# Optimization experiments

Measured on AMD Instinct MI355X. Metric: run time of the kernel, lower is better.

Reference implementation:

```python
import jax, jax.numpy as jnp
import numpy as np

C = 256   # hidden_size (in_channels)
V = 97    # VOC_SIZE + 1
T = 32    # encoder time steps
N = 4096  # batch of text instances


def setup_inputs() -> dict:
    key = jax.random.key(0)
    ks = jax.random.split(key, 10)
    s = lambda k, shape: jax.random.normal(k, shape, dtype=jnp.float32) * 0.05
    return {
        "input": jax.random.randint(ks[0], (N,), 0, V),
        "hidden": s(ks[1], (1, N, C)),
        "encoder_outputs": s(ks[2], (T, N, C)),
        "emb": s(ks[3], (V, C)),
        "combine_w": s(ks[4], (C, 2 * C)), "combine_b": jnp.zeros((C,), jnp.float32),
        "vat_w": s(ks[5], (1, C)), "vat_b": jnp.zeros((1,), jnp.float32),
        "gru_w_ih": s(ks[6], (3 * C, C)), "gru_w_hh": s(ks[7], (3 * C, C)),
        "gru_b_ih": jnp.zeros((3 * C,), jnp.float32), "gru_b_hh": jnp.zeros((3 * C,), jnp.float32),
        "out_w": s(ks[8], (V, C)), "out_b": jnp.zeros((V,), jnp.float32),
    }


def reference(input, hidden, encoder_outputs, emb, combine_w, combine_b,
              vat_w, vat_b, gru_w_ih, gru_w_hh, gru_b_ih, gru_b_hh,
              out_w, out_b):
    # Embedding lookup (dropout = identity in eval mode)
    embedded = emb[input]                                   # [N, C]

    # Bahdanau additive attention: vat(tanh(hidden + enc))
    alpha = jnp.tanh(hidden + encoder_outputs)              # [T, N, C]
    scores = jnp.einsum('tnc,c->nt', alpha, vat_w[0]) + vat_b[0]  # [N, T]
    attn = jax.nn.softmax(scores, axis=1)                   # [N, T]
    applied = jnp.einsum('nt,tnc->nc', attn, encoder_outputs)     # [N, C]

    # Combine + relu
    x = jnp.concatenate([embedded, applied], axis=1) @ combine_w.T + combine_b  # [N, C]
    x = jax.nn.relu(x)

    # Single-step GRU cell (PyTorch gate ordering: r, z, n)
    h = hidden[0]                                           # [N, C]
    gi = x @ gru_w_ih.T + gru_b_ih                          # [N, 3C]
    gh = h @ gru_w_hh.T + gru_b_hh                          # [N, 3C]
    ir, iz, i_n = jnp.split(gi, 3, axis=1)
    hr, hz, h_n = jnp.split(gh, 3, axis=1)
    r = jax.nn.sigmoid(ir + hr)
    z = jax.nn.sigmoid(iz + hz)
    n = jnp.tanh(i_n + r * h_n)
    h_new = (1.0 - z) * n + z * h                           # [N, C]

    out = jax.nn.log_softmax(h_new @ out_w.T + out_b, axis=1)  # [N, V]
    return out, h_new[None, :, :], attn[:, None, :]
```

## Files before the change

### kernel.cpp

```cpp
#include <hip/hip_runtime.h>

typedef unsigned short u16;
typedef unsigned int u32;
using bf16x8 = __attribute__((ext_vector_type(8))) __bf16;
using f32x4  = __attribute__((ext_vector_type(4))) float;

__device__ __forceinline__ u16 f2bf(float f) {
  union { float f; unsigned int i; } v; v.f = f;
  unsigned int r = v.i + 0x7fffu + ((v.i >> 16) & 1u);
  return (u16)(r >> 16);
}
__device__ __forceinline__ void cvt8(u16* dst, const float* src) {
  float4 a0 = *reinterpret_cast<const float4*>(src);
  float4 a1 = *reinterpret_cast<const float4*>(src + 4);
  dst[0] = f2bf(a0.x); dst[1] = f2bf(a0.y); dst[2] = f2bf(a0.z); dst[3] = f2bf(a0.w);
  dst[4] = f2bf(a1.x); dst[5] = f2bf(a1.y); dst[6] = f2bf(a1.z); dst[7] = f2bf(a1.w);
}
__device__ __forceinline__ float ftanh(float x) {
  float e = __expf(2.f * x);
  return 1.f - 2.f / (e + 1.f);
}
__device__ __forceinline__ float fsigm(float x) {
  return 1.f / (1.f + __expf(-x));
}
__device__ __forceinline__ float ptanh(float x) {
  const float c1 = -0.3333333333f, c2 = 0.1333333333f, c3 = -0.0539682540f;
  float t = x * x;
  float r = __builtin_fmaf(__builtin_fmaf(c3, t, c2), t, c1);
  return __builtin_fmaf(x * t, r, x);
}

__global__ __launch_bounds__(512) void k_attn(
    const float* __restrict__ enc, const float* __restrict__ hid,
    const float* __restrict__ vw,
    const float* __restrict__ emb, const int* __restrict__ inp,
    float* __restrict__ attn_out, u16* __restrict__ Acomb)
{
  __shared__ float es_s[16 * 33];
  __shared__ float l_s[16];

  const int tid = threadIdx.x;
  const int nl  = tid >> 5;
  const int cg  = tid & 31;
  const int c0  = cg * 8;
  const int n   = blockIdx.x * 16 + nl;

  const float4 h0 = *reinterpret_cast<const float4*>(&hid[n * 256 + c0]);
  const float4 h1 = *reinterpret_cast<const float4*>(&hid[n * 256 + c0 + 4]);
  const float4 w0 = *reinterpret_cast<const float4*>(&vw[c0]);
  const float4 w1 = *reinterpret_cast<const float4*>(&vw[c0 + 4]);

  float a0=0.f,a1=0.f,a2=0.f,a3=0.f,a4=0.f,a5=0.f,a6=0.f,a7=0.f;
  float l = 0.f;

  const float* ep = &enc[(size_t)n * 256 + c0];
  #pragma unroll 4
  for (int t = 0; t < 32; ++t) {
    const float* p = ep + (size_t)t * 1048576;
    float4 e0 = *reinterpret_cast<const float4*>(p);
    float4 e1 = *reinterpret_cast<const float4*>(p + 4);

    float s;
    s  = ptanh(h0.x + e0.x) * w0.x;
    s  = __builtin_fmaf(ptanh(h0.y + e0.y), w0.y, s);
    s  = __builtin_fmaf(ptanh(h0.z + e0.z), w0.z, s);
    s  = __builtin_fmaf(ptanh(h0.w + e0.w), w0.w, s);
    s  = __builtin_fmaf(ptanh(h1.x + e1.x), w1.x, s);
    s  = __builtin_fmaf(ptanh(h1.y + e1.y), w1.y, s);
    s  = __builtin_fmaf(ptanh(h1.z + e1.z), w1.z, s);
    s  = __builtin_fmaf(ptanh(h1.w + e1.w), w1.w, s);
    #pragma unroll
    for (int k = 16; k >= 1; k >>= 1) s += __shfl_xor(s, k, 64);

    float e = __expf(s);
    l += e;
    a0 = __builtin_fmaf(e, e0.x, a0); a1 = __builtin_fmaf(e, e0.y, a1);
    a2 = __builtin_fmaf(e, e0.z, a2); a3 = __builtin_fmaf(e, e0.w, a3);
    a4 = __builtin_fmaf(e, e1.x, a4); a5 = __builtin_fmaf(e, e1.y, a5);
    a6 = __builtin_fmaf(e, e1.z, a6); a7 = __builtin_fmaf(e, e1.w, a7);
    if (cg == 0) es_s[nl * 33 + t] = e;
  }

  {
    float rl = 1.f / l;
    u16 tmp[8];
    tmp[0]=f2bf(a0*rl); tmp[1]=f2bf(a1*rl); tmp[2]=f2bf(a2*rl); tmp[3]=f2bf(a3*rl);
    tmp[4]=f2bf(a4*rl); tmp[5]=f2bf(a5*rl); tmp[6]=f2bf(a6*rl); tmp[7]=f2bf(a7*rl);
    *reinterpret_cast<uint4*>(&Acomb[n * 512 + 256 + c0]) =
      *reinterpret_cast<const uint4*>(tmp);
  }
  {
    int row = inp[n];
    u16 tmp[8];
    cvt8(tmp, &emb[row * 256 + c0]);
    *reinterpret_cast<uint4*>(&Acomb[n * 512 + c0]) =
      *reinterpret_cast<const uint4*>(tmp);
  }
  if (cg == 0) l_s[nl] = l;
  __syncthreads();

  {
    int n2 = tid >> 5, t2 = tid & 31;
    attn_out[(blockIdx.x * 16 + n2) * 32 + t2] = es_s[n2 * 33 + t2] / l_s[n2];
  }
}

__global__ __launch_bounds__(256) void k_combine(
    const u16* __restrict__ A, const float* __restrict__ W,
    const float* __restrict__ bias, u16* __restrict__ X)
{
  __shared__ u16 As[64 * 40];
  __shared__ u16 Bs[64 * 40];

  const int tid = threadIdx.x;
  const int lane = tid & 63;
  const int wave = tid >> 6;
  const int lr = lane & 15, quad = lane >> 4;
  const int m0 = blockIdx.x * 64;
  const int j0 = blockIdx.y * 64;
  const int wm = (wave & 1) * 32;
  const int wn = (wave >> 1) * 32;
  const int sr = tid >> 2, sq = tid & 3;

  f32x4 acc[2][2] = {};

  for (int kt = 0; kt < 16; ++kt) {
    int k0 = kt * 32;
    *reinterpret_cast<uint4*>(&As[sr * 40 + sq * 8]) =
      *reinterpret_cast<const uint4*>(&A[(m0 + sr) * 512 + k0 + sq * 8]);
    cvt8(&Bs[sr * 40 + sq * 8], &W[(j0 + sr) * 512 + k0 + sq * 8]);
    __syncthreads();
    bf16x8 aF[2], bF[2];
    #pragma unroll
    for (int s = 0; s < 2; ++s) {
      aF[s] = *reinterpret_cast<const bf16x8*>(&As[(wm + s * 16 + lr) * 40 + quad * 8]);
      bF[s] = *reinterpret_cast<const bf16x8*>(&Bs[(wn + s * 16 + lr) * 40 + quad * 8]);
    }
    #pragma unroll
    for (int sm = 0; sm < 2; ++sm)
      #pragma unroll
      for (int sn = 0; sn < 2; ++sn)
        acc[sm][sn] = __builtin_amdgcn_mfma_f32_16x16x32_bf16(aF[sm], bF[sn], acc[sm][sn], 0, 0, 0);
    __syncthreads();
  }

  #pragma unroll
  for (int sm = 0; sm < 2; ++sm) {
    #pragma unroll
    for (int sn = 0; sn < 2; ++sn) {
      int gc = j0 + wn + sn * 16 + lr;
      float bv = bias[gc];
      int gr = m0 + wm + sm * 16 + quad * 4;
      #pragma unroll
      for (int r = 0; r < 4; ++r) {
        float v = acc[sm][sn][r] + bv;
        X[(gr + r) * 256 + gc] = f2bf(fmaxf(v, 0.f));
      }
    }
  }
}

__global__ __launch_bounds__(256) void k_gru(
    const u16* __restrict__ X, const float* __restrict__ Hin,
    const float* __restrict__ Wih, const float* __restrict__ Whh,
    const float* __restrict__ bih, const float* __restrict__ bhh,
    float* __restrict__ Hout)
{
  __shared__ u16 Xs[64 * 40];
  __shared__ u16 Hs[64 * 40];
  __shared__ u16 Bs[6 * 32 * 40];

  const int tid = threadIdx.x;
  const int lane = tid & 63;
  const int wave = tid >> 6;
  const int lr = lane & 15, quad = lane >> 4;
  const int m0 = blockIdx.x * 64;
  const int c0 = blockIdx.y * 32;

  f32x4 aI[3][2] = {};
  f32x4 aH[3][2] = {};

  for (int kt = 0; kt < 8; ++kt) {
    int k0 = kt * 32;
    for (int ci = tid; ci < 1280; ci += 256) {
      if (ci < 256) {
        int r = ci >> 2, q = ci & 3;
        *reinterpret_cast<uint4*>(&Xs[r * 40 + q * 8]) =
          *reinterpret_cast<const uint4*>(&X[(m0 + r) * 256 + k0 + q * 8]);
      } else if (ci < 512) {
        int b = ci - 256;
        int r = b >> 2, q = b & 3;
        cvt8(&Hs[r * 40 + q * 8], &Hin[(m0 + r) * 256 + k0 + q * 8]);
      } else {
        int b = ci - 512;
        int g = b >> 7, r = (b >> 2) & 31, q = b & 3;
        const float* Wsrc = (g < 3) ? Wih : Whh;
        int gg = (g < 3) ? g : g - 3;
        cvt8(&Bs[(g * 32 + r) * 40 + q * 8],
             &Wsrc[(gg * 256 + c0 + r) * 256 + k0 + q * 8]);
      }
    }
    __syncthreads();
    bf16x8 xF = *reinterpret_cast<const bf16x8*>(&Xs[(wave * 16 + lr) * 40 + quad * 8]);
    bf16x8 hF = *reinterpret_cast<const bf16x8*>(&Hs[(wave * 16 + lr) * 40 + quad * 8]);
    #pragma unroll
    for (int g = 0; g < 3; ++g) {
      #pragma unroll
      for (int sn = 0; sn < 2; ++sn) {
        bf16x8 bI = *reinterpret_cast<const bf16x8*>(&Bs[(g * 32 + sn * 16 + lr) * 40 + quad * 8]);
        bf16x8 bH = *reinterpret_cast<const bf16x8*>(&Bs[((g + 3) * 32 + sn * 16 + lr) * 40 + quad * 8]);
        aI[g][sn] = __builtin_amdgcn_mfma_f32_16x16x32_bf16(xF, bI, aI[g][sn], 0, 0, 0);
        aH[g][sn] = __builtin_amdgcn_mfma_f32_16x16x32_bf16(hF, bH, aH[g][sn], 0, 0, 0);
      }
    }
    __syncthreads();
  }

  #pragma unroll
  for (int sn = 0; sn < 2; ++sn) {
    int gc = c0 + sn * 16 + lr;
    float b_ir = bih[gc],       b_hr = bhh[gc];
    float b_iz = bih[256 + gc], b_hz = bhh[256 + gc];
    float b_in = bih[512 + gc], b_hn = bhh[512 + gc];
    #pragma unroll
    for (int r = 0; r < 4; ++r) {
      int grow = m0 + wave * 16 + quad * 4 + r;
      float rg = fsigm(aI[0][sn][r] + b_ir + aH[0][sn][r] + b_hr);
      float zg = fsigm(aI[1][sn][r] + b_iz + aH[1][sn][r] + b_hz);
      float ng = ftanh(aI[2][sn][r] + b_in + rg * (aH[2][sn][r] + b_hn));
      float hv = Hin[grow * 256 + gc];
      Hout[grow * 256 + gc] = (1.f - zg) * ng + zg * hv;
    }
  }
}

__global__ __launch_bounds__(256) void k_out(
    const float* __restrict__ H, const float* __restrict__ Wo,
    const float* __restrict__ bo, float* __restrict__ O)
{
  __shared__ u16 As[32 * 40];
  __shared__ u16 Bs[128 * 40];
  __shared__ float L[32 * 101];
  __shared__ float pm[32 * 8], pl[32 * 8];
  __shared__ float lz_s[32];

  const int tid = threadIdx.x;
  const int lane = tid & 63;
  const int wave = tid >> 6;
  const int lr = lane & 15, quad = lane >> 4;
  const int m0 = blockIdx.x * 32;
  const int rg = (wave >> 1) * 16;
  const int sg = (wave & 1) * 4;

  for (int i = tid; i < 128 * 40; i += 256) { if ((i / 40) >= 97) Bs[i] = 0; }

  f32x4 acc[4] = {};

  for (int kt = 0; kt < 8; ++kt) {
    int k0 = kt * 32;
    if (tid < 128) {
      int r = tid >> 2, q = tid & 3;
      cvt8(&As[r * 40 + q * 8], &H[(m0 + r) * 256 + k0 + q * 8]);
    }
    #pragma unroll
    for (int it = 0; it < 2; ++it) {
      int ci = tid + it * 256;
      int br = ci >> 2, bq = ci & 3;
      if (br < 97)
        cvt8(&Bs[br * 40 + bq * 8], &Wo[br * 256 + k0 + bq * 8]);
    }
    __syncthreads();
    bf16x8 aF = *reinterpret_cast<const bf16x8*>(&As[(rg + lr) * 40 + quad * 8]);
    #pragma unroll
    for (int s = 0; s < 4; ++s) {
      bf16x8 bF = *reinterpret_cast<const bf16x8*>(&Bs[((sg + s) * 16 + lr) * 40 + quad * 8]);
      acc[s] = __builtin_amdgcn_mfma_f32_16x16x32_bf16(aF, bF, acc[s], 0, 0, 0);
    }
    __syncthreads();
  }

  #pragma unroll
  for (int s = 0; s < 4; ++s) {
    int col = (sg + s) * 16 + lr;
    if (col < 97) {
      float bv = bo[col];
      #pragma unroll
      for (int r = 0; r < 4; ++r)
        L[(rg + quad * 4 + r) * 101 + col] = acc[s][r] + bv;
    }
  }
  __syncthreads();

  {
    int row = tid >> 3, p = tid & 7;
    float m = -1e30f, l = 0.f;
    for (int c = p; c < 97; c += 8) {
      float v = L[row * 101 + c];
      if (v > m) { l = l * __expf(m - v) + 1.f; m = v; }
      else l += __expf(v - m);
    }
    pm[row * 8 + p] = m; pl[row * 8 + p] = l;
  }
  __syncthreads();

  if (tid < 32) {
    float M = -1e30f;
    #pragma unroll
    for (int p = 0; p < 8; ++p) M = fmaxf(M, pm[tid * 8 + p]);
    float S = 0.f;
    #pragma unroll
    for (int p = 0; p < 8; ++p) S += pl[tid * 8 + p] * __expf(pm[tid * 8 + p] - M);
    lz_s[tid] = M + __logf(S);
  }
  __syncthreads();

  {
    int row = tid >> 3, p = tid & 7;
    float lz = lz_s[row];
    for (int c = p; c < 97; c += 8)
      O[(m0 + row) * 97 + c] = L[row * 101 + c] - lz;
  }
}

extern "C" void kernel_launch(void* const* d_in, const int* in_sizes, int n_in,
                              void* d_out, int out_size, void* d_ws, size_t ws_size,
                              hipStream_t stream) {
  const int*   inp = (const int*)d_in[0];
  const float* hid = (const float*)d_in[1];
  const float* enc = (const float*)d_in[2];
  const float* emb = (const float*)d_in[3];
  const float* cw  = (const float*)d_in[4];
  const float* cb  = (const float*)d_in[5];
  const float* vw  = (const float*)d_in[6];
  const float* wih = (const float*)d_in[8];
  const float* whh = (const float*)d_in[9];
  const float* bih = (const float*)d_in[10];
  const float* bhh = (const float*)d_in[11];
  const float* ow  = (const float*)d_in[12];
  const float* ob  = (const float*)d_in[13];

  float* out        = (float*)d_out;
  float* out_logits = out;
  float* out_h      = out + 4096 * 97;
  float* out_attn   = out_h + 4096 * 256;

  u16* Acomb = (u16*)d_ws;
  u16* Xbuf  = Acomb + 4096 * 512;

  k_attn<<<256, 512, 0, stream>>>(enc, hid, vw, emb, inp, out_attn, Acomb);
  k_combine<<<dim3(64, 4), 256, 0, stream>>>(Acomb, cw, cb, Xbuf);
  k_gru<<<dim3(64, 8), 256, 0, stream>>>(Xbuf, hid, wih, whh, bih, bhh, out_h);
  k_out<<<128, 256, 0, stream>>>(out_h, ow, ob, out_logits);
}
```

Baseline: 279.1 us.

## Fuse attention, combine, GRU and output projection into one per-tile kernel

Replaces the four kernels (attention, combine GEMM, GRU GEMM, output log-softmax) with a weight pre-conversion kernel plus one fused kernel. Each 16-row block keeps its intermediates (embedding+context, relu output, new hidden) in shared memory as bf16 and reads pre-converted bf16 weights straight from global memory. This removes the global round trips for the intermediate activations, three kernel launches, and the repeated per-tile fp32-to-bf16 weight conversion. The cost is that every block re-reads the full weight matrices from L2 without sharing them through LDS, and only 256 blocks run the GEMM phases with small M tiles.

```diff
diff --git a/kernel.cpp b/kernel.cpp
--- a/kernel.cpp
+++ b/kernel.cpp
@@ -30,295 +30,240 @@
   return __builtin_fmaf(x * t, r, x);
 }
 
-__global__ __launch_bounds__(512) void k_attn(
+__global__ __launch_bounds__(256) void k_prep(
+    const float* __restrict__ cw, const float* __restrict__ wih,
+    const float* __restrict__ whh, const float* __restrict__ ow,
+    u16* __restrict__ Wc, u16* __restrict__ Wi,
+    u16* __restrict__ Wh, u16* __restrict__ Wo)
+{
+  int id = blockIdx.x * 256 + threadIdx.x;
+  u16 tmp[8];
+  if (id < 16384) {
+    cvt8(tmp, &cw[id * 8]);
+    *reinterpret_cast<uint4*>(&Wc[id * 8]) = *reinterpret_cast<const uint4*>(tmp);
+  } else if (id < 40960) {
+    int c = id - 16384;
+    cvt8(tmp, &wih[c * 8]);
+    *reinterpret_cast<uint4*>(&Wi[c * 8]) = *reinterpret_cast<const uint4*>(tmp);
+  } else if (id < 65536) {
+    int c = id - 40960;
+    cvt8(tmp, &whh[c * 8]);
+    *reinterpret_cast<uint4*>(&Wh[c * 8]) = *reinterpret_cast<const uint4*>(tmp);
+  } else {
+    int c = id - 65536;
+    int row = c >> 5, col = (c & 31) * 8;
+    if (row < 97) {
+      cvt8(tmp, &ow[row * 256 + col]);
+    } else {
+      #pragma unroll
+      for (int i = 0; i < 8; ++i) tmp[i] = 0;
+    }
+    *reinterpret_cast<uint4*>(&Wo[c * 8]) = *reinterpret_cast<const uint4*>(tmp);
+  }
+}
+
+__global__ __launch_bounds__(512) void k_fused(
     const float* __restrict__ enc, const float* __restrict__ hid,
-    const float* __restrict__ vw,
-    const float* __restrict__ emb, const int* __restrict__ inp,
-    float* __restrict__ attn_out, u16* __restrict__ Acomb)
+    const float* __restrict__ vw,  const float* __restrict__ emb,
+    const int* __restrict__ inp,
+    const u16* __restrict__ Wc, const u16* __restrict__ Wi,
+    const u16* __restrict__ Wh, const u16* __restrict__ Wo,
+    const float* __restrict__ cb, const float* __restrict__ bih,
+    const float* __restrict__ bhh, const float* __restrict__ bo,
+    float* __restrict__ out_logits, float* __restrict__ out_h,
+    float* __restrict__ out_attn)
 {
+  __shared__ __attribute__((aligned(16))) u16 Ac_s[16 * 16 * 40];
+  __shared__ __attribute__((aligned(16))) u16 Hb_s[8 * 16 * 40];
+  __shared__ __attribute__((aligned(16))) u16 X_s [8 * 16 * 40];
+  __shared__ __attribute__((aligned(16))) u16 Hn_s[8 * 16 * 40];
   __shared__ float es_s[16 * 33];
   __shared__ float l_s[16];
+  __shared__ float L_s[16 * 113];
 
   const int tid = threadIdx.x;
-  const int nl  = tid >> 5;
-  const int cg  = tid & 31;
-  const int c0  = cg * 8;
-  const int n   = blockIdx.x * 16 + nl;
-
-  const float4 h0 = *reinterpret_cast<const float4*>(&hid[n * 256 + c0]);
-  const float4 h1 = *reinterpret_cast<const float4*>(&hid[n * 256 + c0 + 4]);
-  const float4 w0 = *reinterpret_cast<const float4*>(&vw[c0]);
-  const float4 w1 = *reinterpret_cast<const float4*>(&vw[c0 + 4]);
-
-  float a0=0.f,a1=0.f,a2=0.f,a3=0.f,a4=0.f,a5=0.f,a6=0.f,a7=0.f;
-  float l = 0.f;
-
-  const float* ep = &enc[(size_t)n * 256 + c0];
-  #pragma unroll 4
-  for (int t = 0; t < 32; ++t) {
-    const float* p = ep + (size_t)t * 1048576;
-    float4 e0 = *reinterpret_cast<const float4*>(p);
-    float4 e1 = *reinterpret_cast<const float4*>(p + 4);
-
-    float s;
-    s  = ptanh(h0.x + e0.x) * w0.x;
-    s  = __builtin_fmaf(ptanh(h0.y + e0.y), w0.y, s);
-    s  = __builtin_fmaf(ptanh(h0.z + e0.z), w0.z, s);
-    s  = __builtin_fmaf(ptanh(h0.w + e0.w), w0.w, s);
-    s  = __builtin_fmaf(ptanh(h1.x + e1.x), w1.x, s);
-    s  = __builtin_fmaf(ptanh(h1.y + e1.y), w1.y, s);
-    s  = __builtin_fmaf(ptanh(h1.z + e1.z), w1.z, s);
-    s  = __builtin_fmaf(ptanh(h1.w + e1.w), w1.w, s);
-    #pragma unroll
-    for (int k = 16; k >= 1; k >>= 1) s += __shfl_xor(s, k, 64);
-
-    float e = __expf(s);
-    l += e;
-    a0 = __builtin_fmaf(e, e0.x, a0); a1 = __builtin_fmaf(e, e0.y, a1);
-    a2 = __builtin_fmaf(e, e0.z, a2); a3 = __builtin_fmaf(e, e0.w, a3);
-    a4 = __builtin_fmaf(e, e1.x, a4); a5 = __builtin_fmaf(e, e1.y, a5);
-    a6 = __builtin_fmaf(e, e1.z, a6); a7 = __builtin_fmaf(e, e1.w, a7);
-    if (cg == 0) es_s[nl * 33 + t] = e;
-  }
-
-  {
-    float rl = 1.f / l;
-    u16 tmp[8];
-    tmp[0]=f2bf(a0*rl); tmp[1]=f2bf(a1*rl); tmp[2]=f2bf(a2*rl); tmp[3]=f2bf(a3*rl);
-    tmp[4]=f2bf(a4*rl); tmp[5]=f2bf(a5*rl); tmp[6]=f2bf(a6*rl); tmp[7]=f2bf(a7*rl);
-    *reinterpret_cast<uint4*>(&Acomb[n * 512 + 256 + c0]) =
-      *reinterpret_cast<const uint4*>(tmp);
-  }
-  {
-    int row = inp[n];
-    u16 tmp[8];
-    cvt8(tmp, &emb[row * 256 + c0]);
-    *reinterpret_cast<uint4*>(&Acomb[n * 512 + c0]) =
-      *reinterpret_cast<const uint4*>(tmp);
-  }
-  if (cg == 0) l_s[nl] = l;
+  const int n0  = blockIdx.x * 16;
+
+  {
+    const int nl = tid >> 5;
+    const int cg = tid & 31;
+    const int c0 = cg * 8;
+    const int n  = n0 + nl;
+
+    const float4 h0 = *reinterpret_cast<const float4*>(&hid[n * 256 + c0]);
+    const float4 h1 = *reinterpret_cast<const float4*>(&hid[n * 256 + c0 + 4]);
+    const float4 w0 = *reinterpret_cast<const float4*>(&vw[c0]);
+    const float4 w1 = *reinterpret_cast<const float4*>(&vw[c0 + 4]);
+
+    {
+      u16 t8[8];
+      t8[0]=f2bf(h0.x); t8[1]=f2bf(h0.y); t8[2]=f2bf(h0.z); t8[3]=f2bf(h0.w);
+      t8[4]=f2bf(h1.x); t8[5]=f2bf(h1.y); t8[6]=f2bf(h1.z); t8[7]=f2bf(h1.w);
+      *reinterpret_cast<uint4*>(&Hb_s[((cg >> 2) * 16 + nl) * 40 + (cg & 3) * 8]) =
+        *reinterpret_cast<const uint4*>(t8);
+    }
+    {
+      u16 t8[8];
+      cvt8(t8, &emb[(size_t)inp[n] * 256 + c0]);
+      *reinterpret_cast<uint4*>(&Ac_s[((cg >> 2) * 16 + nl) * 40 + (cg & 3) * 8]) =
+        *reinterpret_cast<const uint4*>(t8);
+    }
+
+    float a0=0.f,a1=0.f,a2=0.f,a3=0.f,a4=0.f,a5=0.f,a6=0.f,a7=0.f;
+    float l = 0.f;
+
+    const float* ep = &enc[(size_t)n * 256 + c0];
+    #pragma unroll 4
+    for (int t = 0; t < 32; ++t) {
+      const float* p = ep + (size_t)t * 1048576;
+      float4 e0 = *reinterpret_cast<const float4*>(p);
+      float4 e1 = *reinterpret_cast<const float4*>(p + 4);
+
+      float s;
+      s  = ptanh(h0.x + e0.x) * w0.x;
+      s  = __builtin_fmaf(ptanh(h0.y + e0.y), w0.y, s);
+      s  = __builtin_fmaf(ptanh(h0.z + e0.z), w0.z, s);
+      s  = __builtin_fmaf(ptanh(h0.w + e0.w), w0.w, s);
+      s  = __builtin_fmaf(ptanh(h1.x + e1.x), w1.x, s);
+      s  = __builtin_fmaf(ptanh(h1.y + e1.y), w1.y, s);
+      s  = __builtin_fmaf(ptanh(h1.z + e1.z), w1.z, s);
+      s  = __builtin_fmaf(ptanh(h1.w + e1.w), w1.w, s);
+      #pragma unroll
+      for (int k = 16; k >= 1; k >>= 1) s += __shfl_xor(s, k, 64);
+
+      float e = __expf(s);
+      l += e;
+      a0 = __builtin_fmaf(e, e0.x, a0); a1 = __builtin_fmaf(e, e0.y, a1);
+      a2 = __builtin_fmaf(e, e0.z, a2); a3 = __builtin_fmaf(e, e0.w, a3);
+      a4 = __builtin_fmaf(e, e1.x, a4); a5 = __builtin_fmaf(e, e1.y, a5);
+      a6 = __builtin_fmaf(e, e1.z, a6); a7 = __builtin_fmaf(e, e1.w, a7);
+      if (cg == 0) es_s[nl * 33 + t] = e;
+    }
+
+    {
+      float rl = 1.f / l;
+      u16 t8[8];
+      t8[0]=f2bf(a0*rl); t8[1]=f2bf(a1*rl); t8[2]=f2bf(a2*rl); t8[3]=f2bf(a3*rl);
+      t8[4]=f2bf(a4*rl); t8[5]=f2bf(a5*rl); t8[6]=f2bf(a6*rl); t8[7]=f2bf(a7*rl);
+      *reinterpret_cast<uint4*>(&Ac_s[((8 + (cg >> 2)) * 16 + nl) * 40 + (cg & 3) * 8]) =
+        *reinterpret_cast<const uint4*>(t8);
+    }
+    if (cg == 0) l_s[nl] = l;
+  }
   __syncthreads();
 
   {
     int n2 = tid >> 5, t2 = tid & 31;
-    attn_out[(blockIdx.x * 16 + n2) * 32 + t2] = es_s[n2 * 33 + t2] / l_s[n2];
-  }
-}
-
-__global__ __launch_bounds__(256) void k_combine(
-    const u16* __restrict__ A, const float* __restrict__ W,
-    const float* __restrict__ bias, u16* __restrict__ X)
-{
-  __shared__ u16 As[64 * 40];
-  __shared__ u16 Bs[64 * 40];
-
-  const int tid = threadIdx.x;
-  const int lane = tid & 63;
-  const int wave = tid >> 6;
+    out_attn[(size_t)(n0 + n2) * 32 + t2] = es_s[n2 * 33 + t2] / l_s[n2];
+  }
+
+  const int wave = tid >> 6, lane = tid & 63;
   const int lr = lane & 15, quad = lane >> 4;
-  const int m0 = blockIdx.x * 64;
-  const int j0 = blockIdx.y * 64;
-  const int wm = (wave & 1) * 32;
-  const int wn = (wave >> 1) * 32;
-  const int sr = tid >> 2, sq = tid & 3;
-
-  f32x4 acc[2][2] = {};
-
-  for (int kt = 0; kt < 16; ++kt) {
-    int k0 = kt * 32;
-    *reinterpret_cast<uint4*>(&As[sr * 40 + sq * 8]) =
-      *reinterpret_cast<const uint4*>(&A[(m0 + sr) * 512 + k0 + sq * 8]);
-    cvt8(&Bs[sr * 40 + sq * 8], &W[(j0 + sr) * 512 + k0 + sq * 8]);
-    __syncthreads();
-    bf16x8 aF[2], bF[2];
-    #pragma unroll
-    for (int s = 0; s < 2; ++s) {
-      aF[s] = *reinterpret_cast<const bf16x8*>(&As[(wm + s * 16 + lr) * 40 + quad * 8]);
-      bF[s] = *reinterpret_cast<const bf16x8*>(&Bs[(wn + s * 16 + lr) * 40 + quad * 8]);
-    }
-    #pragma unroll
-    for (int sm = 0; sm < 2; ++sm)
-      #pragma unroll
-      for (int sn = 0; sn < 2; ++sn)
-        acc[sm][sn] = __builtin_amdgcn_mfma_f32_16x16x32_bf16(aF[sm], bF[sn], acc[sm][sn], 0, 0, 0);
-    __syncthreads();
-  }
-
-  #pragma unroll
-  for (int sm = 0; sm < 2; ++sm) {
+
+  {
+    f32x4 accB[2] = {};
+    const u16* wp = &Wc[(size_t)(wave * 32 + lr) * 512 + quad * 8];
+    #pragma unroll
+    for (int kt = 0; kt < 16; ++kt) {
+      bf16x8 aF = *reinterpret_cast<const bf16x8*>(&Ac_s[(kt * 16 + lr) * 40 + quad * 8]);
+      bf16x8 b0 = *reinterpret_cast<const bf16x8*>(&wp[kt * 32]);
+      bf16x8 b1 = *reinterpret_cast<const bf16x8*>(&wp[16 * 512 + kt * 32]);
+      accB[0] = __builtin_amdgcn_mfma_f32_16x16x32_bf16(aF, b0, accB[0], 0, 0, 0);
+      accB[1] = __builtin_amdgcn_mfma_f32_16x16x32_bf16(aF, b1, accB[1], 0, 0, 0);
+    }
     #pragma unroll
     for (int sn = 0; sn < 2; ++sn) {
-      int gc = j0 + wn + sn * 16 + lr;
-      float bv = bias[gc];
-      int gr = m0 + wm + sm * 16 + quad * 4;
+      int col = wave * 32 + sn * 16 + lr;
+      float bv = cb[col];
       #pragma unroll
       for (int r = 0; r < 4; ++r) {
-        float v = acc[sm][sn][r] + bv;
-        X[(gr + r) * 256 + gc] = f2bf(fmaxf(v, 0.f));
+        float v = fmaxf(accB[sn][r] + bv, 0.f);
+        X_s[((col >> 5) * 16 + quad * 4 + r) * 40 + (col & 31)] = f2bf(v);
       }
     }
   }
-}
-
-__global__ __launch_bounds__(256) void k_gru(
-    const u16* __restrict__ X, const float* __restrict__ Hin,
-    const float* __restrict__ Wih, const float* __restrict__ Whh,
-    const float* __restrict__ bih, const float* __restrict__ bhh,
-    float* __restrict__ Hout)
-{
-  __shared__ u16 Xs[64 * 40];
-  __shared__ u16 Hs[64 * 40];
-  __shared__ u16 Bs[6 * 32 * 40];
-
-  const int tid = threadIdx.x;
-  const int lane = tid & 63;
-  const int wave = tid >> 6;
-  const int lr = lane & 15, quad = lane >> 4;
-  const int m0 = blockIdx.x * 64;
-  const int c0 = blockIdx.y * 32;
-
-  f32x4 aI[3][2] = {};
-  f32x4 aH[3][2] = {};
-
-  for (int kt = 0; kt < 8; ++kt) {
-    int k0 = kt * 32;
-    for (int ci = tid; ci < 1280; ci += 256) {
-      if (ci < 256) {
-        int r = ci >> 2, q = ci & 3;
-        *reinterpret_cast<uint4*>(&Xs[r * 40 + q * 8]) =
-          *reinterpret_cast<const uint4*>(&X[(m0 + r) * 256 + k0 + q * 8]);
-      } else if (ci < 512) {
-        int b = ci - 256;
-        int r = b >> 2, q = b & 3;
-        cvt8(&Hs[r * 40 + q * 8], &Hin[(m0 + r) * 256 + k0 + q * 8]);
-      } else {
-        int b = ci - 512;
-        int g = b >> 7, r = (b >> 2) & 31, q = b & 3;
-        const float* Wsrc = (g < 3) ? Wih : Whh;
-        int gg = (g < 3) ? g : g - 3;
-        cvt8(&Bs[(g * 32 + r) * 40 + q * 8],
-             &Wsrc[(gg * 256 + c0 + r) * 256 + k0 + q * 8]);
+  __syncthreads();
+
+  {
+    f32x4 aI[3][2] = {};
+    f32x4 aH[3][2] = {};
+    const int c0w = wave * 32;
+    const u16* baseI = &Wi[(size_t)(c0w + lr) * 256 + quad * 8];
+    const u16* baseH = &Wh[(size_t)(c0w + lr) * 256 + quad * 8];
+    #pragma unroll
+    for (int kt = 0; kt < 8; ++kt) {
+      bf16x8 xF = *reinterpret_cast<const bf16x8*>(&X_s [(kt * 16 + lr) * 40 + quad * 8]);
+      bf16x8 hF = *reinterpret_cast<const bf16x8*>(&Hb_s[(kt * 16 + lr) * 40 + quad * 8]);
+      #pragma unroll
+      for (int g = 0; g < 3; ++g) {
+        #pragma unroll
+        for (int sn = 0; sn < 2; ++sn) {
+          const size_t off = (size_t)(g * 256 + sn * 16) * 256 + kt * 32;
+          bf16x8 bI = *reinterpret_cast<const bf16x8*>(&baseI[off]);
+          bf16x8 bH = *reinterpret_cast<const bf16x8*>(&baseH[off]);
+          aI[g][sn] = __builtin_amdgcn_mfma_f32_16x16x32_bf16(xF, bI, aI[g][sn], 0, 0, 0);
+          aH[g][sn] = __builtin_amdgcn_mfma_f32_16x16x32_bf16(hF, bH, aH[g][sn], 0, 0, 0);
+        }
       }
     }
-    __syncthreads();
-    bf16x8 xF = *reinterpret_cast<const bf16x8*>(&Xs[(wave * 16 + lr) * 40 + quad * 8]);
-    bf16x8 hF = *reinterpret_cast<const bf16x8*>(&Hs[(wave * 16 + lr) * 40 + quad * 8]);
-    #pragma unroll
-    for (int g = 0; g < 3; ++g) {
-      #pragma unroll
-      for (int sn = 0; sn < 2; ++sn) {
-        bf16x8 bI = *reinterpret_cast<const bf16x8*>(&Bs[(g * 32 + sn * 16 + lr) * 40 + quad * 8]);
-        bf16x8 bH = *reinterpret_cast<const bf16x8*>(&Bs[((g + 3) * 32 + sn * 16 + lr) * 40 + quad * 8]);
-        aI[g][sn] = __builtin_amdgcn_mfma_f32_16x16x32_bf16(xF, bI, aI[g][sn], 0, 0, 0);
-        aH[g][sn] = __builtin_amdgcn_mfma_f32_16x16x32_bf16(hF, bH, aH[g][sn], 0, 0, 0);
+    #pragma unroll
+    for (int sn = 0; sn < 2; ++sn) {
+      int gc = c0w + sn * 16 + lr;
+      float b_ir = bih[gc],       b_hr = bhh[gc];
+      float b_iz = bih[256 + gc], b_hz = bhh[256 + gc];
+      float b_in = bih[512 + gc], b_hn = bhh[512 + gc];
+      #pragma unroll
+      for (int r = 0; r < 4; ++r) {
+        int row = quad * 4 + r;
+        float rg = fsigm(aI[0][sn][r] + b_ir + aH[0][sn][r] + b_hr);
+        float zg = fsigm(aI[1][sn][r] + b_iz + aH[1][sn][r] + b_hz);
+        float ng = ftanh(aI[2][sn][r] + b_in + rg * (aH[2][sn][r] + b_hn));
+        float hv = hid[(size_t)(n0 + row) * 256 + gc];
+        float hn = (1.f - zg) * ng + zg * hv;
+        out_h[(size_t)(n0 + row) * 256 + gc] = hn;
+        Hn_s[((gc >> 5) * 16 + row) * 40 + (gc & 31)] = f2bf(hn);
       }
     }
-    __syncthreads();
-  }
-
-  #pragma unroll
-  for (int sn = 0; sn < 2; ++sn) {
-    int gc = c0 + sn * 16 + lr;
-    float b_ir = bih[gc],       b_hr = bhh[gc];
-    float b_iz = bih[256 + gc], b_hz = bhh[256 + gc];
-    float b_in = bih[512 + gc], b_hn = bhh[512 + gc];
-    #pragma unroll
-    for (int r = 0; r < 4; ++r) {
-      int grow = m0 + wave * 16 + quad * 4 + r;
-      float rg = fsigm(aI[0][sn][r] + b_ir + aH[0][sn][r] + b_hr);
-      float zg = fsigm(aI[1][sn][r] + b_iz + aH[1][sn][r] + b_hz);
-      float ng = ftanh(aI[2][sn][r] + b_in + rg * (aH[2][sn][r] + b_hn));
-      float hv = Hin[grow * 256 + gc];
-      Hout[grow * 256 + gc] = (1.f - zg) * ng + zg * hv;
-    }
-  }
-}
-
-__global__ __launch_bounds__(256) void k_out(
-    const float* __restrict__ H, const float* __restrict__ Wo,
-    const float* __restrict__ bo, float* __restrict__ O)
-{
-  __shared__ u16 As[32 * 40];
-  __shared__ u16 Bs[128 * 40];
-  __shared__ float L[32 * 101];
-  __shared__ float pm[32 * 8], pl[32 * 8];
-  __shared__ float lz_s[32];
-
-  const int tid = threadIdx.x;
-  const int lane = tid & 63;
-  const int wave = tid >> 6;
-  const int lr = lane & 15, quad = lane >> 4;
-  const int m0 = blockIdx.x * 32;
-  const int rg = (wave >> 1) * 16;
-  const int sg = (wave & 1) * 4;
-
-  for (int i = tid; i < 128 * 40; i += 256) { if ((i / 40) >= 97) Bs[i] = 0; }
-
-  f32x4 acc[4] = {};
-
-  for (int kt = 0; kt < 8; ++kt) {
-    int k0 = kt * 32;
-    if (tid < 128) {
-      int r = tid >> 2, q = tid & 3;
-      cvt8(&As[r * 40 + q * 8], &H[(m0 + r) * 256 + k0 + q * 8]);
-    }
-    #pragma unroll
-    for (int it = 0; it < 2; ++it) {
-      int ci = tid + it * 256;
-      int br = ci >> 2, bq = ci & 3;
-      if (br < 97)
-        cvt8(&Bs[br * 40 + bq * 8], &Wo[br * 256 + k0 + bq * 8]);
-    }
-    __syncthreads();
-    bf16x8 aF = *reinterpret_cast<const bf16x8*>(&As[(rg + lr) * 40 + quad * 8]);
-    #pragma unroll
-    for (int s = 0; s < 4; ++s) {
-      bf16x8 bF = *reinterpret_cast<const bf16x8*>(&Bs[((sg + s) * 16 + lr) * 40 + quad * 8]);
-      acc[s] = __builtin_amdgcn_mfma_f32_16x16x32_bf16(aF, bF, acc[s], 0, 0, 0);
-    }
-    __syncthreads();
-  }
-
-  #pragma unroll
-  for (int s = 0; s < 4; ++s) {
-    int col = (sg + s) * 16 + lr;
+  }
+  __syncthreads();
+
+  if (wave < 7) {
+    f32x4 accO = {};
+    const u16* wp = &Wo[(size_t)(wave * 16 + lr) * 256 + quad * 8];
+    #pragma unroll
+    for (int kt = 0; kt < 8; ++kt) {
+      bf16x8 aF = *reinterpret_cast<const bf16x8*>(&Hn_s[(kt * 16 + lr) * 40 + quad * 8]);
+      bf16x8 bF = *reinterpret_cast<const bf16x8*>(&wp[kt * 32]);
+      accO = __builtin_amdgcn_mfma_f32_16x16x32_bf16(aF, bF, accO, 0, 0, 0);
+    }
+    int col = wave * 16 + lr;
     if (col < 97) {
       float bv = bo[col];
       #pragma unroll
       for (int r = 0; r < 4; ++r)
-        L[(rg + quad * 4 + r) * 101 + col] = acc[s][r] + bv;
+        L_s[(quad * 4 + r) * 113 + col] = accO[r] + bv;
     }
   }
   __syncthreads();
 
   {
-    int row = tid >> 3, p = tid & 7;
+    int row = tid >> 5, p = tid & 31;
     float m = -1e30f, l = 0.f;
-    for (int c = p; c < 97; c += 8) {
-      float v = L[row * 101 + c];
+    for (int c = p; c < 97; c += 32) {
+      float v = L_s[row * 113 + c];
       if (v > m) { l = l * __expf(m - v) + 1.f; m = v; }
       else l += __expf(v - m);
     }
-    pm[row * 8 + p] = m; pl[row * 8 + p] = l;
-  }
-  __syncthreads();
-
-  if (tid < 32) {
-    float M = -1e30f;
-    #pragma unroll
-    for (int p = 0; p < 8; ++p) M = fmaxf(M, pm[tid * 8 + p]);
-    float S = 0.f;
-    #pragma unroll
-    for (int p = 0; p < 8; ++p) S += pl[tid * 8 + p] * __expf(pm[tid * 8 + p] - M);
-    lz_s[tid] = M + __logf(S);
-  }
-  __syncthreads();
-
-  {
-    int row = tid >> 3, p = tid & 7;
-    float lz = lz_s[row];
-    for (int c = p; c < 97; c += 8)
-      O[(m0 + row) * 97 + c] = L[row * 101 + c] - lz;
+    #pragma unroll
+    for (int k = 16; k >= 1; k >>= 1) {
+      float m2 = __shfl_xor(m, k, 64);
+      float l2 = __shfl_xor(l, k, 64);
+      if (m2 > m) { l = l * __expf(m - m2) + l2; m = m2; }
+      else l += l2 * __expf(m2 - m);
+    }
+    float lz = m + __logf(l);
+    for (int c = p; c < 97; c += 32)
+      out_logits[(size_t)(n0 + row) * 97 + c] = L_s[row * 113 + c] - lz;
   }
 }
 
@@ -344,11 +289,13 @@
   float* out_h      = out + 4096 * 97;
   float* out_attn   = out_h + 4096 * 256;
 
-  u16* Acomb = (u16*)d_ws;
-  u16* Xbuf  = Acomb + 4096 * 512;
-
-  k_attn<<<256, 512, 0, stream>>>(enc, hid, vw, emb, inp, out_attn, Acomb);
-  k_combine<<<dim3(64, 4), 256, 0, stream>>>(Acomb, cw, cb, Xbuf);
-  k_gru<<<dim3(64, 8), 256, 0, stream>>>(Xbuf, hid, wih, whh, bih, bhh, out_h);
-  k_out<<<128, 256, 0, stream>>>(out_h, ow, ob, out_logits);
-}
+  u16* Wc = (u16*)d_ws;
+  u16* Wi = Wc + 131072;
+  u16* Wh = Wi + 196608;
+  u16* Wo = Wh + 196608;
+
+  k_prep<<<270, 256, 0, stream>>>(cw, wih, whh, ow, Wc, Wi, Wh, Wo);
+  k_fused<<<256, 512, 0, stream>>>(enc, hid, vw, emb, inp,
+                                   Wc, Wi, Wh, Wo, cb, bih, bhh, ob,
+                                   out_logits, out_h, out_attn);
+}
```

Result: faster. 253.5 us (-9.2%).
